# Kernel tuning notes

Measured on AMD Instinct MI355X. Metric: run time of the kernel, lower is better.

Reference implementation:

```python
import jax, jax.numpy as jnp
import numpy as np

N_NODES = 100000
N_EDGES = 1600000
FEATURE_DIM, CONDITION_DIM, HIDDEN_DIM, LATENT_DIM = 256, 64, 128, 64


def setup_inputs() -> dict:
    key = jax.random.key(0)
    ks = jax.random.split(key, 12)

    def glorot(k, fan_in, fan_out):
        s = np.sqrt(6.0 / (fan_in + fan_out)).astype(np.float32)
        return jax.random.uniform(k, (fan_in, fan_out), jnp.float32, -s, s)

    return {
        "feature": jax.random.normal(ks[0], (N_NODES, FEATURE_DIM), jnp.float32),
        "condition": jax.random.normal(ks[1], (N_NODES, CONDITION_DIM), jnp.float32),
        "edge_index": jax.random.randint(ks[2], (2, N_EDGES), 0, N_NODES, jnp.int64),
        "W_f2h": glorot(ks[3], FEATURE_DIM, HIDDEN_DIM),
        "b_f2h": jnp.zeros((HIDDEN_DIM,), jnp.float32),
        "W_c2h": glorot(ks[4], CONDITION_DIM, HIDDEN_DIM),
        "b_c2h": jnp.zeros((HIDDEN_DIM,), jnp.float32),
        "W_h2h": glorot(ks[5], 2 * HIDDEN_DIM, HIDDEN_DIM),
        "b_h2h": jnp.zeros((HIDDEN_DIM,), jnp.float32),
        "W_h2l": glorot(ks[6], HIDDEN_DIM, LATENT_DIM),
        "b_h2l": jnp.zeros((LATENT_DIM,), jnp.float32),
    }


def reference(feature, condition, edge_index, W_f2h, b_f2h, W_c2h, b_c2h,
              W_h2h, b_h2h, W_h2l, b_h2l):
    N = feature.shape[0]
    self_loops = jnp.arange(N, dtype=edge_index.dtype)
    src = jnp.concatenate([edge_index[0], self_loops])  # message sources (j)
    dst = jnp.concatenate([edge_index[1], self_loops])  # message targets (i)

    # symmetric GCN normalization: D^{-1/2} (A+I) D^{-1/2}
    deg = jax.ops.segment_sum(jnp.ones(dst.shape[0], feature.dtype), dst,
                              num_segments=N)
    dinv = jnp.where(deg > 0, jax.lax.rsqrt(deg), 0.0)
    norm = dinv[src] * dinv[dst]  # [E+N]

    def gcn_conv(x, W, b):
        xl = x @ W                                   # [N, out]
        msg = xl[src] * norm[:, None]                # gather + scale
        return jax.ops.segment_sum(msg, dst, num_segments=N) + b

    f2h = jnp.tanh(gcn_conv(feature, W_f2h, b_f2h))
    c2h = jnp.tanh(gcn_conv(condition, W_c2h, b_c2h))
    h = jnp.concatenate([f2h, c2h], axis=1)          # [N, 2*hidden]
    h = jnp.tanh(gcn_conv(h, W_h2h, b_h2h))
    z = gcn_conv(h, W_h2l, b_h2l)
    return z
```

## Files before the change

### kernel.cpp

```cpp
#include <hip/hip_runtime.h>
#include <cmath>
#include <cstdint>


typedef _Float16 f16;
typedef _Float16 f16x8 __attribute__((ext_vector_type(8)));
typedef float f32x4 __attribute__((ext_vector_type(4)));

__global__ void count_zero_kernel(int* __restrict__ count, int N) {
    int i = blockIdx.x * 256 + threadIdx.x;
    if (i < N) count[i] = 0;
}

__global__ void count_kernel(const int* __restrict__ dst, int* __restrict__ count, int E) {
    int e = blockIdx.x * 256 + threadIdx.x;
    if (e < E) atomicAdd(&count[dst[e]], 1);
}

__global__ void dinv_kernel(const int* __restrict__ count, float* __restrict__ dinv, int N) {
    int i = blockIdx.x * 256 + threadIdx.x;
    if (i < N) dinv[i] = rsqrtf((float)(count[i] + 1));
}

constexpr int SCAN_VPT = 8;
constexpr int SCAN_TILE = 256 * SCAN_VPT;

__global__ __launch_bounds__(256) void scan_partial_kernel(const int* __restrict__ count,
                                                           int* __restrict__ blocksums, int N) {
    __shared__ int red[256];
    const int t = threadIdx.x;
    int base = blockIdx.x * SCAN_TILE + t * SCAN_VPT;
    int s = 0;
#pragma unroll
    for (int i = 0; i < SCAN_VPT; ++i) {
        int idx = base + i;
        if (idx < N) s += count[idx];
    }
    red[t] = s;
    __syncthreads();
    for (int off = 128; off > 0; off >>= 1) {
        if (t < off) red[t] += red[t + off];
        __syncthreads();
    }
    if (t == 0) blocksums[blockIdx.x] = red[0];
}

__global__ __launch_bounds__(1024) void scan_blocksums_kernel(int* __restrict__ blocksums, int nb) {
    __shared__ int sh[1024];
    const int t = threadIdx.x;
    int v = (t < nb) ? blocksums[t] : 0;
    sh[t] = v;
    __syncthreads();
    for (int off = 1; off < 1024; off <<= 1) {
        int u = (t >= off) ? sh[t - off] : 0;
        __syncthreads();
        sh[t] += u;
        __syncthreads();
    }
    if (t < nb) blocksums[t] = sh[t] - v;
}

__global__ __launch_bounds__(256) void scan_final_kernel(const int* __restrict__ count,
                                                         const int* __restrict__ blocksums,
                                                         int* __restrict__ row_ptr,
                                                         int* __restrict__ cursor, int N) {
    __shared__ int red[256];
    const int t = threadIdx.x;
    int base = blockIdx.x * SCAN_TILE + t * SCAN_VPT;
    int vals[SCAN_VPT];
    int s = 0;
#pragma unroll
    for (int i = 0; i < SCAN_VPT; ++i) {
        int idx = base + i;
        vals[i] = (idx < N) ? count[idx] : 0;
        s += vals[i];
    }
    red[t] = s;
    __syncthreads();
    for (int off = 1; off < 256; off <<= 1) {
        int u = (t >= off) ? red[t - off] : 0;
        __syncthreads();
        red[t] += u;
        __syncthreads();
    }
    int run = red[t] - s + blocksums[blockIdx.x];
#pragma unroll
    for (int i = 0; i < SCAN_VPT; ++i) {
        int idx = base + i;
        if (idx < N) {
            row_ptr[idx] = run;
            cursor[idx] = 0;
            run += vals[i];
            if (idx == N - 1) row_ptr[N] = run;
        }
    }
}

__global__ void fill_kernel(const int* __restrict__ src, const int* __restrict__ dst,
                            const float* __restrict__ dinv, const int* __restrict__ row_ptr,
                            int* __restrict__ cursor, int2* __restrict__ csr, int E) {
    int e = blockIdx.x * 256 + threadIdx.x;
    if (e >= E) return;
    int s = src[e];
    int d = dst[e];
    int pos = row_ptr[d] + atomicAdd(&cursor[d], 1);
    float nrm = dinv[s] * dinv[d];
    csr[pos] = make_int2(s, __float_as_int(nrm));
}

__global__ void wprep_kernel(const float* __restrict__ W, f16* __restrict__ wt_hi,
                             f16* __restrict__ wt_lo, int K, int M) {
    int idx = blockIdx.x * 256 + threadIdx.x;
    if (idx >= K * M) return;
    int k = idx / M, m = idx % M;
    float w = W[idx];
    f16 h = (f16)w;
    wt_hi[(size_t)m * K + k] = h;
    wt_lo[(size_t)m * K + k] = (f16)(w - (float)h);
}

__global__ void f32to16_kernel(const float* __restrict__ x, f16* __restrict__ y, int n4) {
    int i = blockIdx.x * 256 + threadIdx.x;
    if (i < n4) {
        float4 v = ((const float4*)x)[i];
        union { f16 h[4]; uint2 u; } p;
        p.h[0] = (f16)v.x; p.h[1] = (f16)v.y; p.h[2] = (f16)v.z; p.h[3] = (f16)v.w;
        ((uint2*)y)[i] = p.u;
    }
}

template <int K, int M, bool BIAS_TANH, bool X_IS_HALF>
__global__ __launch_bounds__(256) void gemm_mfma_kernel(
    const void* __restrict__ Xv, const f16* __restrict__ Wth,
    const f16* __restrict__ Wtl, const float* __restrict__ bias,
    f16* __restrict__ out, int ld, int colOff, int N) {
    constexpr int BM = 128, BK = 32, XP = 40;
    constexpr int CT = M / 16;
    __shared__ f16 xs[BM * XP];
    __shared__ f16 whs[M * XP];
    __shared__ f16 wls[M * XP];

    const int tid = threadIdx.x;
    const int lane = tid & 63;
    const int wv = tid >> 6;
    const int m16 = lane & 15;
    const int quad = lane >> 4;
    const int row0 = blockIdx.x * BM;

    f32x4 acc[2][CT];
#pragma unroll
    for (int rt = 0; rt < 2; ++rt)
#pragma unroll
        for (int ct = 0; ct < CT; ++ct) acc[rt][ct] = (f32x4){0.f, 0.f, 0.f, 0.f};

    for (int k0 = 0; k0 < K; k0 += BK) {
        if (X_IS_HALF) {
            const f16* X = (const f16*)Xv;
#pragma unroll
            for (int i = 0; i < 2; ++i) {
                int c = i * 256 + tid;
                int r = c >> 2, ko = (c & 3) * 8;
                uint4 v = make_uint4(0u, 0u, 0u, 0u);
                if (row0 + r < N) v = *(const uint4*)(X + (size_t)(row0 + r) * K + k0 + ko);
                *(uint4*)(&xs[r * XP + ko]) = v;
            }
        } else {
            const float* X = (const float*)Xv;
#pragma unroll
            for (int i = 0; i < 4; ++i) {
                int c = i * 256 + tid;
                int r = c >> 3, kq = (c & 7) * 4;
                float4 v = make_float4(0.f, 0.f, 0.f, 0.f);
                if (row0 + r < N) v = *(const float4*)(X + (size_t)(row0 + r) * K + k0 + kq);
                union { f16 h[4]; uint2 u; } p;
                p.h[0] = (f16)v.x; p.h[1] = (f16)v.y; p.h[2] = (f16)v.z; p.h[3] = (f16)v.w;
                *(uint2*)(&xs[r * XP + kq]) = p.u;
            }
        }
#pragma unroll
        for (int i = 0; i < (M * 4) / 256; ++i) {
            int c = i * 256 + tid;
            int n = c >> 2, ko = (c & 3) * 8;
            *(uint4*)(&whs[n * XP + ko]) = *(const uint4*)(Wth + (size_t)n * K + k0 + ko);
            *(uint4*)(&wls[n * XP + ko]) = *(const uint4*)(Wtl + (size_t)n * K + k0 + ko);
        }
        __syncthreads();

        f16x8 a0 = *(const f16x8*)(&xs[(wv * 32 + 0 + m16) * XP + quad * 8]);
        f16x8 a1 = *(const f16x8*)(&xs[(wv * 32 + 16 + m16) * XP + quad * 8]);
#pragma unroll
        for (int ct = 0; ct < CT; ++ct) {
            f16x8 bh = *(const f16x8*)(&whs[(ct * 16 + m16) * XP + quad * 8]);
            f16x8 bl = *(const f16x8*)(&wls[(ct * 16 + m16) * XP + quad * 8]);
            acc[0][ct] = __builtin_amdgcn_mfma_f32_16x16x32_f16(a0, bh, acc[0][ct], 0, 0, 0);
            acc[0][ct] = __builtin_amdgcn_mfma_f32_16x16x32_f16(a0, bl, acc[0][ct], 0, 0, 0);
            acc[1][ct] = __builtin_amdgcn_mfma_f32_16x16x32_f16(a1, bh, acc[1][ct], 0, 0, 0);
            acc[1][ct] = __builtin_amdgcn_mfma_f32_16x16x32_f16(a1, bl, acc[1][ct], 0, 0, 0);
        }
        __syncthreads();
    }

    float brs[CT];
    if (BIAS_TANH) {
#pragma unroll
        for (int ct = 0; ct < CT; ++ct) brs[ct] = bias[ct * 16 + m16];
    }

#pragma unroll
    for (int rt = 0; rt < 2; ++rt) {
#pragma unroll
        for (int r = 0; r < 4; ++r) {
            int row = row0 + wv * 32 + rt * 16 + quad * 4 + r;
            if (row < N) {
                f16* op = out + (size_t)row * ld + colOff + m16;
#pragma unroll
                for (int ct = 0; ct < CT; ++ct) {
                    float v = acc[rt][ct][r];
                    if (BIAS_TANH) v = tanhf(v + brs[ct]);
                    op[ct * 16] = (f16)v;
                }
            }
        }
    }
}

template <int M, bool TANH, bool HAS_BIAS, bool OUT_F32>
__global__ __launch_bounds__(256) void gather_h_kernel(
    const f16* __restrict__ xl, const float* __restrict__ b,
    const float* __restrict__ dinv, const int* __restrict__ row_ptr,
    const int2* __restrict__ csr, void* __restrict__ outv,
    int ld, int colOff, int N) {
    constexpr int TPN = M / 8;
    int gid = blockIdx.x * 256 + threadIdx.x;
    int node = gid / TPN;
    int t = gid % TPN;
    if (node >= N) return;

    float di = dinv[node];
    float self = di * di;
    f16x8 x = *(const f16x8*)(xl + (size_t)node * M + t * 8);
    float acc[8];
#pragma unroll
    for (int j = 0; j < 8; ++j) acc[j] = (float)x[j] * self;
    if (HAS_BIAS) {
        float4 b0 = *(const float4*)(b + t * 8);
        float4 b1 = *(const float4*)(b + t * 8 + 4);
        acc[0] += b0.x; acc[1] += b0.y; acc[2] += b0.z; acc[3] += b0.w;
        acc[4] += b1.x; acc[5] += b1.y; acc[6] += b1.z; acc[7] += b1.w;
    }

    int p = row_ptr[node];
    const int p1 = row_ptr[node + 1];
    for (; p + 2 <= p1; p += 2) {
        int2 e0 = csr[p];
        int2 e1 = csr[p + 1];
        f16x8 v0 = *(const f16x8*)(xl + (size_t)e0.x * M + t * 8);
        f16x8 v1 = *(const f16x8*)(xl + (size_t)e1.x * M + t * 8);
        float n0 = __int_as_float(e0.y);
        float n1 = __int_as_float(e1.y);
#pragma unroll
        for (int j = 0; j < 8; ++j) acc[j] += (float)v0[j] * n0 + (float)v1[j] * n1;
    }
    if (p < p1) {
        int2 e0 = csr[p];
        f16x8 v0 = *(const f16x8*)(xl + (size_t)e0.x * M + t * 8);
        float n0 = __int_as_float(e0.y);
#pragma unroll
        for (int j = 0; j < 8; ++j) acc[j] += (float)v0[j] * n0;
    }

    if (TANH) {
#pragma unroll
        for (int j = 0; j < 8; ++j) acc[j] = tanhf(acc[j]);
    }

    if (OUT_F32) {
        float* op = (float*)outv + (size_t)node * ld + colOff + t * 8;
        *(float4*)op = make_float4(acc[0], acc[1], acc[2], acc[3]);
        *(float4*)(op + 4) = make_float4(acc[4], acc[5], acc[6], acc[7]);
    } else {
        f16x8 o;
#pragma unroll
        for (int j = 0; j < 8; ++j) o[j] = (f16)acc[j];
        *(f16x8*)((f16*)outv + (size_t)node * ld + colOff + t * 8) = o;
    }
}

extern "C" void kernel_launch(void* const* d_in, const int* in_sizes, int n_in,
                              void* d_out, int out_size, void* d_ws, size_t ws_size,
                              hipStream_t stream) {
    const int FD = 256;

    const float* feature   = (const float*)d_in[0];
    const float* condition = (const float*)d_in[1];
    const int*   edge      = (const int*)d_in[2];
    const float* W_f2h = (const float*)d_in[3];
    const float* b_f2h = (const float*)d_in[4];
    const float* W_c2h = (const float*)d_in[5];
    const float* b_c2h = (const float*)d_in[6];
    const float* W_h2h = (const float*)d_in[7];
    const float* b_h2h = (const float*)d_in[8];
    const float* W_h2l = (const float*)d_in[9];
    const float* b_h2l = (const float*)d_in[10];
    float* out = (float*)d_out;

    const int N = in_sizes[0] / FD;
    const int E = in_sizes[2] / 2;
    const int* src = edge;
    const int* dst = edge + E;

    float* ws_f   = (float*)d_ws;
    float* dinv   = ws_f;
    int*   count  = (int*)(ws_f + N);
    int*   rowp   = count + N;
    int*   cursor = rowp + N + 1;
    int*   bsums  = cursor + N;
    int2*  csr    = (int2*)(((uintptr_t)(bsums + 1024) + 15) & ~(uintptr_t)15);
    f16*   A_h    = (f16*)(csr + E);
    f16*   B_h    = A_h + (size_t)N * 128;
    f16*   cond_h = B_h + (size_t)N * 256;
    f16*   wt1h   = cond_h + (size_t)N * 64;
    f16*   wt1l   = wt1h + 128 * 256;
    f16*   wt2h   = wt1l + 128 * 256;
    f16*   wt2l   = wt2h + 128 * 64;
    f16*   wt3h   = wt2l + 128 * 64;
    f16*   wt3l   = wt3h + 128 * 256;
    f16*   wt4h   = wt3l + 128 * 256;
    f16*   wt4l   = wt4h + 64 * 128;

    const int TB = 256;
    dim3 blk(TB);
    const int nScanBlocks = (N + SCAN_TILE - 1) / SCAN_TILE;

    wprep_kernel<<<(256 * 128 + TB - 1) / TB, blk, 0, stream>>>(W_f2h, wt1h, wt1l, 256, 128);
    wprep_kernel<<<(64 * 128 + TB - 1) / TB, blk, 0, stream>>>(W_c2h, wt2h, wt2l, 64, 128);
    wprep_kernel<<<(256 * 128 + TB - 1) / TB, blk, 0, stream>>>(W_h2h, wt3h, wt3l, 256, 128);
    wprep_kernel<<<(128 * 64 + TB - 1) / TB, blk, 0, stream>>>(W_h2l, wt4h, wt4l, 128, 64);
    f32to16_kernel<<<(N * 16 + TB - 1) / TB, blk, 0, stream>>>(condition, cond_h, N * 16);

    count_zero_kernel<<<(N + TB - 1) / TB, blk, 0, stream>>>(count, N);
    count_kernel<<<(E + TB - 1) / TB, blk, 0, stream>>>(dst, count, E);
    dinv_kernel<<<(N + TB - 1) / TB, blk, 0, stream>>>(count, dinv, N);
    scan_partial_kernel<<<nScanBlocks, blk, 0, stream>>>(count, bsums, N);
    scan_blocksums_kernel<<<1, 1024, 0, stream>>>(bsums, nScanBlocks);
    scan_final_kernel<<<nScanBlocks, blk, 0, stream>>>(count, bsums, rowp, cursor, N);
    fill_kernel<<<(E + TB - 1) / TB, blk, 0, stream>>>(src, dst, dinv, rowp, cursor, csr, E);

    const int gemm_grid = (N + 127) / 128;
    const int g128 = (N * 16 + TB - 1) / TB;
    const int g64  = (N * 8 + TB - 1) / TB;

    gemm_mfma_kernel<256, 128, false, false><<<gemm_grid, blk, 0, stream>>>(
        feature, wt1h, wt1l, nullptr, A_h, 128, 0, N);
    gather_h_kernel<128, true, true, false><<<g128, blk, 0, stream>>>(
        A_h, b_f2h, dinv, rowp, csr, B_h, 256, 0, N);

    gather_h_kernel<64, false, false, false><<<g64, blk, 0, stream>>>(
        cond_h, nullptr, dinv, rowp, csr, A_h, 64, 0, N);
    gemm_mfma_kernel<64, 128, true, true><<<gemm_grid, blk, 0, stream>>>(
        A_h, wt2h, wt2l, b_c2h, B_h, 256, 128, N);

    gemm_mfma_kernel<256, 128, false, true><<<gemm_grid, blk, 0, stream>>>(
        B_h, wt3h, wt3l, nullptr, A_h, 128, 0, N);
    gather_h_kernel<128, true, true, false><<<g128, blk, 0, stream>>>(
        A_h, b_h2h, dinv, rowp, csr, B_h, 128, 0, N);

    gemm_mfma_kernel<128, 64, false, true><<<gemm_grid, blk, 0, stream>>>(
        B_h, wt4h, wt4l, nullptr, A_h, 64, 0, N);
    gather_h_kernel<64, false, true, true><<<g64, blk, 0, stream>>>(
        A_h, b_h2l, dinv, rowp, csr, out, 64, 0, N);
}
```

Baseline: 759.7 us.

## Split GEMM waves by output columns and unroll gather loop by four

The MFMA GEMM now gives each wave a quarter of the output columns across all 128 rows of the tile. Each wave loads its W fragments from shared memory once per K step into registers and reuses them across eight row tiles, where before every wave read all W columns. The CSR gather loop is unrolled from two to four neighbors, so more independent row loads are in flight per thread. The trade-off is higher register pressure from larger accumulator and B-fragment arrays, plus more A-fragment LDS reads per wave.

After: 757.2 us. About the same (-0.3%).

```diff
diff --git a/kernel.cpp b/kernel.cpp
--- a/kernel.cpp
+++ b/kernel.cpp
@@ -135,7 +135,9 @@
     const f16* __restrict__ Wtl, const float* __restrict__ bias,
     f16* __restrict__ out, int ld, int colOff, int N) {
     constexpr int BM = 128, BK = 32, XP = 40;
-    constexpr int CT = M / 16;
+    constexpr int SW = M / 4;
+    constexpr int CT = SW / 16;
+    constexpr int RT = BM / 16;
     __shared__ f16 xs[BM * XP];
     __shared__ f16 whs[M * XP];
     __shared__ f16 wls[M * XP];
@@ -147,9 +149,9 @@
     const int quad = lane >> 4;
     const int row0 = blockIdx.x * BM;
 
-    f32x4 acc[2][CT];
-#pragma unroll
-    for (int rt = 0; rt < 2; ++rt)
+    f32x4 acc[RT][CT];
+#pragma unroll
+    for (int rt = 0; rt < RT; ++rt)
 #pragma unroll
         for (int ct = 0; ct < CT; ++ct) acc[rt][ct] = (f32x4){0.f, 0.f, 0.f, 0.f};
 
@@ -186,16 +188,20 @@
         }
         __syncthreads();
 
-        f16x8 a0 = *(const f16x8*)(&xs[(wv * 32 + 0 + m16) * XP + quad * 8]);
-        f16x8 a1 = *(const f16x8*)(&xs[(wv * 32 + 16 + m16) * XP + quad * 8]);
+        f16x8 bh[CT], bl[CT];
 #pragma unroll
         for (int ct = 0; ct < CT; ++ct) {
-            f16x8 bh = *(const f16x8*)(&whs[(ct * 16 + m16) * XP + quad * 8]);
-            f16x8 bl = *(const f16x8*)(&wls[(ct * 16 + m16) * XP + quad * 8]);
-            acc[0][ct] = __builtin_amdgcn_mfma_f32_16x16x32_f16(a0, bh, acc[0][ct], 0, 0, 0);
-            acc[0][ct] = __builtin_amdgcn_mfma_f32_16x16x32_f16(a0, bl, acc[0][ct], 0, 0, 0);
-            acc[1][ct] = __builtin_amdgcn_mfma_f32_16x16x32_f16(a1, bh, acc[1][ct], 0, 0, 0);
-            acc[1][ct] = __builtin_amdgcn_mfma_f32_16x16x32_f16(a1, bl, acc[1][ct], 0, 0, 0);
+            bh[ct] = *(const f16x8*)(&whs[(wv * SW + ct * 16 + m16) * XP + quad * 8]);
+            bl[ct] = *(const f16x8*)(&wls[(wv * SW + ct * 16 + m16) * XP + quad * 8]);
+        }
+#pragma unroll
+        for (int rt = 0; rt < RT; ++rt) {
+            f16x8 a = *(const f16x8*)(&xs[(rt * 16 + m16) * XP + quad * 8]);
+#pragma unroll
+            for (int ct = 0; ct < CT; ++ct) {
+                acc[rt][ct] = __builtin_amdgcn_mfma_f32_16x16x32_f16(a, bh[ct], acc[rt][ct], 0, 0, 0);
+                acc[rt][ct] = __builtin_amdgcn_mfma_f32_16x16x32_f16(a, bl[ct], acc[rt][ct], 0, 0, 0);
+            }
         }
         __syncthreads();
     }
@@ -203,16 +209,16 @@
     float brs[CT];
     if (BIAS_TANH) {
 #pragma unroll
-        for (int ct = 0; ct < CT; ++ct) brs[ct] = bias[ct * 16 + m16];
-    }
-
-#pragma unroll
-    for (int rt = 0; rt < 2; ++rt) {
+        for (int ct = 0; ct < CT; ++ct) brs[ct] = bias[wv * SW + ct * 16 + m16];
+    }
+
+#pragma unroll
+    for (int rt = 0; rt < RT; ++rt) {
 #pragma unroll
         for (int r = 0; r < 4; ++r) {
-            int row = row0 + wv * 32 + rt * 16 + quad * 4 + r;
+            int row = row0 + rt * 16 + quad * 4 + r;
             if (row < N) {
-                f16* op = out + (size_t)row * ld + colOff + m16;
+                f16* op = out + (size_t)row * ld + colOff + wv * SW + m16;
 #pragma unroll
                 for (int ct = 0; ct < CT; ++ct) {
                     float v = acc[rt][ct][r];
@@ -251,17 +257,25 @@
 
     int p = row_ptr[node];
     const int p1 = row_ptr[node + 1];
-    for (; p + 2 <= p1; p += 2) {
+    for (; p + 4 <= p1; p += 4) {
         int2 e0 = csr[p];
         int2 e1 = csr[p + 1];
+        int2 e2 = csr[p + 2];
+        int2 e3 = csr[p + 3];
         f16x8 v0 = *(const f16x8*)(xl + (size_t)e0.x * M + t * 8);
         f16x8 v1 = *(const f16x8*)(xl + (size_t)e1.x * M + t * 8);
+        f16x8 v2 = *(const f16x8*)(xl + (size_t)e2.x * M + t * 8);
+        f16x8 v3 = *(const f16x8*)(xl + (size_t)e3.x * M + t * 8);
         float n0 = __int_as_float(e0.y);
         float n1 = __int_as_float(e1.y);
-#pragma unroll
-        for (int j = 0; j < 8; ++j) acc[j] += (float)v0[j] * n0 + (float)v1[j] * n1;
-    }
-    if (p < p1) {
+        float n2 = __int_as_float(e2.y);
+        float n3 = __int_as_float(e3.y);
+#pragma unroll
+        for (int j = 0; j < 8; ++j)
+            acc[j] += ((float)v0[j] * n0 + (float)v1[j] * n1) +
+                      ((float)v2[j] * n2 + (float)v3[j] * n3);
+    }
+    for (; p < p1; ++p) {
         int2 e0 = csr[p];
         f16x8 v0 = *(const f16x8*)(xl + (size_t)e0.x * M + t * 8);
         float n0 = __int_as_float(e0.y);
```
